# Kernel optimization log

Hardware: AMD Instinct MI355X
Metric: run time of the kernel (lower is better)

## Reference

```python
import jax, jax.numpy as jnp
import numpy as np
from jax import lax

EPS = 2e-5      # BatchNorm eps from source
TCLIP = 1.3     # FastSign STE clip


def fast_sign(x):
    # forward: sign(x); backward: grad of clamp(x, -1.3, 1.3) (straight-through)
    c = jnp.clip(x, -TCLIP, TCLIP)
    return lax.stop_gradient(jnp.sign(x) - c) + c


def conv2d(x, w, b, stride, pad):
    y = lax.conv_general_dilated(
        x, w, window_strides=stride,
        padding=[(pad[0], pad[0]), (pad[1], pad[1])],
        dimension_numbers=('NCHW', 'OIHW', 'NCHW'))
    return y + b[None, :, None, None]


def batchnorm(x, g, b):
    # training-mode BN: biased batch stats over (N, H, W)
    m = jnp.mean(x, axis=(0, 2, 3), keepdims=True)
    v = jnp.var(x, axis=(0, 2, 3), keepdims=True)
    return g[None, :, None, None] * (x - m) * lax.rsqrt(v + EPS) + b[None, :, None, None]


def maxpool3x3s2(x):
    return lax.reduce_window(x, -jnp.inf, lax.max, (1, 1, 3, 3), (1, 1, 2, 2), 'VALID')


def setup_inputs() -> dict:
    key = jax.random.key(0)
    ks = jax.random.split(key, 16)
    s = 0.05
    rn = lambda k, shape: jax.random.normal(k, shape, dtype=jnp.float32) * s
    NUM_CLASSES = 1000
    return {
        'x': jax.random.normal(ks[0], (8, 3, 211, 211), dtype=jnp.float32),
        'conv1_w': rn(ks[1], (96, 3, 11, 11)), 'conv1_b': rn(ks[2], (96,)),
        'bn1_g': jnp.ones((96,), jnp.float32), 'bn1_b': jnp.zeros((96,), jnp.float32),
        'conv2_w': rn(ks[3], (256, 96, 5, 5)), 'conv2_b': rn(ks[4], (256,)),
        'bn2_g': jnp.ones((256,), jnp.float32), 'bn2_b': jnp.zeros((256,), jnp.float32),
        'conv3_w': rn(ks[5], (384, 256, 3, 3)), 'conv3_b': rn(ks[6], (384,)),
        'bn3_g': jnp.ones((384,), jnp.float32), 'bn3_b': jnp.zeros((384,), jnp.float32),
        'conv4_w': rn(ks[7], (384, 384, 3, 3)), 'conv4_b': rn(ks[8], (384,)),
        'bn4_g': jnp.ones((384,), jnp.float32), 'bn4_b': jnp.zeros((384,), jnp.float32),
        'conv5_w': rn(ks[9], (256, 384, 3, 3)), 'conv5_b': rn(ks[10], (256,)),
        'bn5_g': jnp.ones((256,), jnp.float32), 'bn5_b': jnp.zeros((256,), jnp.float32),
        'fc1_w': rn(ks[11], (4096, 5)),
        'bn6_g': jnp.ones((256,), jnp.float32), 'bn6_b': jnp.zeros((256,), jnp.float32),
        'fc2_w': rn(ks[12], (4096, 4096)),
        'bn7_g': jnp.ones((256,), jnp.float32), 'bn7_b': jnp.zeros((256,), jnp.float32),
        'fc3_w': rn(ks[13], (NUM_CLASSES, 4096)), 'fc3_b': rn(ks[14], (NUM_CLASSES,)),
    }


def reference(x, conv1_w, conv1_b, bn1_g, bn1_b,
              conv2_w, conv2_b, bn2_g, bn2_b,
              conv3_w, conv3_b, bn3_g, bn3_b,
              conv4_w, conv4_b, bn4_g, bn4_b,
              conv5_w, conv5_b, bn5_g, bn5_b,
              fc1_w, bn6_g, bn6_b,
              fc2_w, bn7_g, bn7_b,
              fc3_w, fc3_b):
    # conv1 (full precision) + BN + relu + pool
    x = conv2d(x, conv1_w, conv1_b, (4, 4), (0, 0))           # [B,96,51,51]
    x = jax.nn.relu(batchnorm(x, bn1_g, bn1_b))
    x = maxpool3x3s2(x)                                        # [B,96,25,25]
    # binary conv blocks (act_q then BinaryConv2d binarizes input again, as in torch)
    x = fast_sign(x)
    x = conv2d(fast_sign(x), fast_sign(conv2_w), conv2_b, (1, 1), (2, 2))  # [B,256,25,25]
    x = batchnorm(x, bn2_g, bn2_b)
    x = maxpool3x3s2(x)                                        # [B,256,12,12]
    x = fast_sign(x)
    x = conv2d(fast_sign(x), fast_sign(conv3_w), conv3_b, (1, 1), (1, 1))  # [B,384,12,12]
    x = batchnorm(x, bn3_g, bn3_b)
    x = fast_sign(x)
    x = conv2d(fast_sign(x), fast_sign(conv4_w), conv4_b, (1, 1), (1, 1))
    x = batchnorm(x, bn4_g, bn4_b)
    x = fast_sign(x)
    x = conv2d(fast_sign(x), fast_sign(conv5_w), conv5_b, (1, 1), (1, 1))  # [B,256,12,12]
    x = batchnorm(x, bn5_g, bn5_b)
    x = maxpool3x3s2(x)                                        # [B,256,5,5]
    # fc layers applied on the LAST dim of the 4D tensor (faithful to torch F.linear)
    x = fast_sign(x)
    x = jnp.matmul(fast_sign(x), fast_sign(fc1_w).T)           # [B,256,5,4096]
    x = jax.nn.relu(batchnorm(x, bn6_g, bn6_b))
    x = fast_sign(x)
    x = jnp.matmul(fast_sign(x), fast_sign(fc2_w).T)           # [B,256,5,4096]
    x = jax.nn.relu(batchnorm(x, bn7_g, bn7_b))
    x = jnp.matmul(x, fc3_w.T) + fc3_b                         # [B,256,5,1000]
    return jax.nn.softmax(x, axis=1)                           # softmax over dim=1 (channels)
```

## Files before the change

### kernel.cpp

```cpp
#include <hip/hip_runtime.h>
#include <cstdint>
#include <cstddef>


typedef int      v4i  __attribute__((ext_vector_type(4)));
typedef float    v4f  __attribute__((ext_vector_type(4)));
typedef _Float16 v8h  __attribute__((ext_vector_type(8)));

#define EPS_BN 2e-5

__device__ __forceinline__ void g2l16(const void* g, void* l) {
  __builtin_amdgcn_global_load_lds((__attribute__((address_space(1))) void*)g,
                                   (__attribute__((address_space(3))) void*)l,
                                   16, 0, 0);
}

__global__ __launch_bounds__(256) void conv1_k(const float* __restrict__ x,
                                               const float* __restrict__ w,
                                               float* __restrict__ y) {
  const int bid = blockIdx.x;
  const int n = bid / 51, oh = bid % 51;
  const int tid = threadIdx.x, lane = tid & 63, wave = tid >> 6;
  __shared__ __align__(16) float xs[3 * 11 * 272];
  for (int i = tid; i < 3 * 11 * 272; i += 256) {
    int iw = i % 272;
    int t = i / 272;
    int kh = t % 11, ci = t / 11;
    float v = 0.f;
    if (iw < 211) v = x[((size_t)(n * 3 + ci) * 211 + (oh * 4 + kh)) * 211 + iw];
    xs[i] = v;
  }
  __syncthreads();
  const int ow = lane;
  const int g = blockIdx.y;
  {
    const int co0 = wave * 24 + g * 4;
    float a0 = 0.f, a1 = 0.f, a2 = 0.f, a3 = 0.f;
    for (int ci = 0; ci < 3; ++ci) {
#pragma unroll
      for (int kh = 0; kh < 11; ++kh) {
        const float* xr = xs + (ci * 11 + kh) * 272 + ow * 4;
        float4 q0 = *(const float4*)(xr);
        float4 q1 = *(const float4*)(xr + 4);
        float4 q2 = *(const float4*)(xr + 8);
        float xv[11] = {q0.x, q0.y, q0.z, q0.w, q1.x, q1.y,
                        q1.z, q1.w, q2.x, q2.y, q2.z};
        const float* wr = w + ((size_t)co0 * 3 + ci) * 121 + kh * 11;
#pragma unroll
        for (int kw = 0; kw < 11; ++kw) {
          float xvv = xv[kw];
          a0 = fmaf(xvv, wr[kw], a0);
          a1 = fmaf(xvv, wr[363 + kw], a1);
          a2 = fmaf(xvv, wr[726 + kw], a2);
          a3 = fmaf(xvv, wr[1089 + kw], a3);
        }
      }
    }
    if (ow < 51) {
      size_t ob = ((size_t)(n * 96 + co0) * 51 + oh) * 51 + ow;
      y[ob] = a0;
      y[ob + 2601] = a1;
      y[ob + 2 * 2601] = a2;
      y[ob + 3 * 2601] = a3;
    }
  }
}

template <typename T>
__global__ __launch_bounds__(256) void bnstat_nchw_k(const T* __restrict__ y,
                                                     const float* __restrict__ g,
                                                     const float* __restrict__ bb,
                                                     float* __restrict__ par,
                                                     int C, int HW, int Nn) {
  const int c = blockIdx.x;
  double s = 0.0, q = 0.0;
  for (int n = 0; n < Nn; ++n) {
    const T* p = y + ((size_t)n * C + c) * HW;
    for (int r = threadIdx.x; r < HW; r += 256) {
      double v = (double)p[r];
      s += v;
      q += v * v;
    }
  }
  __shared__ double ss[256], qq[256];
  ss[threadIdx.x] = s;
  qq[threadIdx.x] = q;
  __syncthreads();
  for (int st = 128; st > 0; st >>= 1) {
    if (threadIdx.x < st) {
      ss[threadIdx.x] += ss[threadIdx.x + st];
      qq[threadIdx.x] += qq[threadIdx.x + st];
    }
    __syncthreads();
  }
  if (threadIdx.x == 0) {
    double P = (double)Nn * HW;
    double m = ss[0] / P, var = qq[0] / P - m * m;
    float inv = (float)(1.0 / sqrt(var + EPS_BN));
    float sc = g[c] * inv;
    par[c] = sc;
    par[512 + c] = bb[c] - (float)m * sc;
  }
}

template <typename T>
__global__ __launch_bounds__(256) void bnstat_nhwc_k(const T* __restrict__ y,
                                                     const float* __restrict__ g,
                                                     const float* __restrict__ bb,
                                                     float* __restrict__ par,
                                                     int C, int P) {
  const int c = blockIdx.x;
  double s = 0.0, q = 0.0;
  for (int p = threadIdx.x; p < P; p += 256) {
    double v = (double)y[(size_t)p * C + c];
    s += v;
    q += v * v;
  }
  __shared__ double ss[256], qq[256];
  ss[threadIdx.x] = s;
  qq[threadIdx.x] = q;
  __syncthreads();
  for (int st = 128; st > 0; st >>= 1) {
    if (threadIdx.x < st) {
      ss[threadIdx.x] += ss[threadIdx.x + st];
      qq[threadIdx.x] += qq[threadIdx.x + st];
    }
    __syncthreads();
  }
  if (threadIdx.x == 0) {
    double Pd = (double)P;
    double m = ss[0] / Pd, var = qq[0] / Pd - m * m;
    float inv = (float)(1.0 / sqrt(var + EPS_BN));
    float sc = g[c] * inv;
    par[c] = sc;
    par[512 + c] = bb[c] - (float)m * sc;
  }
}

__global__ __launch_bounds__(256) void bnp16_k(const short* __restrict__ y,
                                               double* __restrict__ part) {
  const int c = blockIdx.x, n = blockIdx.y;
  const short* p = y + ((size_t)(n * 256 + c)) * 20480;
  long long s = 0, q = 0;
  for (int r = threadIdx.x; r < 20480; r += 256) {
    int v = p[r];
    s += v;
    q += (long long)v * v;
  }
  __shared__ long long ss[256], qq[256];
  ss[threadIdx.x] = s;
  qq[threadIdx.x] = q;
  __syncthreads();
  for (int st = 128; st > 0; st >>= 1) {
    if (threadIdx.x < st) {
      ss[threadIdx.x] += ss[threadIdx.x + st];
      qq[threadIdx.x] += qq[threadIdx.x + st];
    }
    __syncthreads();
  }
  if (threadIdx.x == 0) {
    part[(size_t)(n * 256 + c) * 2] = (double)ss[0];
    part[(size_t)(n * 256 + c) * 2 + 1] = (double)qq[0];
  }
}

__global__ __launch_bounds__(256) void bnf7_k(const double* __restrict__ part,
                                              const float* __restrict__ g,
                                              const float* __restrict__ bb,
                                              float* __restrict__ par) {
  int c = threadIdx.x;
  double s = 0.0, q = 0.0;
  for (int n = 0; n < 8; ++n) {
    s += part[(size_t)(n * 256 + c) * 2];
    q += part[(size_t)(n * 256 + c) * 2 + 1];
  }
  double P = 163840.0;
  double m = s / P, var = q / P - m * m;
  float inv = (float)(1.0 / sqrt(var + EPS_BN));
  float sc = g[c] * inv;
  par[c] = sc;
  par[512 + c] = bb[c] - (float)m * sc;
}

__global__ __launch_bounds__(256) void pool1sign_k(const float* __restrict__ y,
                                                   const float* __restrict__ par,
                                                   int8_t* __restrict__ o) {
  unsigned idx = blockIdx.x * 256 + threadIdx.x;
  if (idx >= 8u * 96 * 25 * 25) return;
  unsigned ow = idx % 25, t = idx / 25;
  unsigned oh = t % 25;
  t /= 25;
  unsigned c = t % 96, n = t / 96;
  float sc = par[c], sh = par[512 + c];
  const float* p = y + ((size_t)(n * 96 + c) * 51 + oh * 2) * 51 + ow * 2;
  float mx = -1e30f, mn = 1e30f;
#pragma unroll
  for (int kh = 0; kh < 3; ++kh)
#pragma unroll
    for (int kw = 0; kw < 3; ++kw) {
      float v = p[kh * 51 + kw];
      mx = fmaxf(mx, v);
      mn = fminf(mn, v);
    }
  float z = (sc >= 0.f ? sc * mx : sc * mn) + sh;
  o[((n * 25 + oh) * 25 + ow) * 96 + c] = (z > 0.f) ? 1 : 0;
}

__global__ __launch_bounds__(256) void poolsign_k(const short* __restrict__ y,
                                                  const float* __restrict__ par,
                                                  int8_t* __restrict__ o, int Nn,
                                                  int Hin, int C, int Hout) {
  unsigned idx = blockIdx.x * 256 + threadIdx.x;
  if (idx >= (unsigned)Nn * Hout * Hout * C) return;
  unsigned c = idx % C;
  unsigned t = idx / C;
  unsigned ow = t % Hout;
  t /= Hout;
  unsigned oh = t % Hout;
  unsigned n = t / Hout;
  const short* p = y + ((size_t)(n * Hin + oh * 2) * Hin + ow * 2) * C + c;
  int mx = -1000000, mn = 1000000;
#pragma unroll
  for (int kh = 0; kh < 3; ++kh)
#pragma unroll
    for (int kw = 0; kw < 3; ++kw) {
      int v = p[(kh * Hin + kw) * C];
      mx = max(mx, v);
      mn = min(mn, v);
    }
  float sc = par[c];
  float z = (sc >= 0.f ? sc * (float)mx : sc * (float)mn) + par[512 + c];
  o[idx] = (z > 0.f) ? 1 : ((z < 0.f) ? -1 : 0);
}

__global__ __launch_bounds__(256) void signk(const short* __restrict__ y,
                                             const float* __restrict__ par,
                                             int8_t* __restrict__ o, int total,
                                             int C) {
  unsigned idx = blockIdx.x * 256 + threadIdx.x;
  if (idx >= (unsigned)total) return;
  unsigned c = idx % C;
  float z = par[c] * (float)y[idx] + par[512 + c];
  o[idx] = (z > 0.f) ? 1 : ((z < 0.f) ? -1 : 0);
}

__global__ __launch_bounds__(256) void pool5sign_k(const short* __restrict__ y,
                                                   const float* __restrict__ par,
                                                   int8_t* __restrict__ o) {
  unsigned idx = blockIdx.x * 256 + threadIdx.x;
  if (idx >= 8u * 256 * 25) return;
  unsigned ow = idx % 5;
  unsigned t = idx / 5;
  unsigned oh = t % 5;
  t /= 5;
  unsigned c = t % 256, n = t / 256;
  const short* p = y + ((size_t)(n * 12 + oh * 2) * 12 + ow * 2) * 256 + c;
  int mx = -1000000, mn = 1000000;
#pragma unroll
  for (int kh = 0; kh < 3; ++kh)
#pragma unroll
    for (int kw = 0; kw < 3; ++kw) {
      int v = p[(kh * 12 + kw) * 256];
      mx = max(mx, v);
      mn = min(mn, v);
    }
  float sc = par[c];
  float z = (sc >= 0.f ? sc * (float)mx : sc * (float)mn) + par[512 + c];
  o[idx] = (z > 0.f) ? 1 : ((z < 0.f) ? -1 : 0);
}

__global__ __launch_bounds__(256) void quantw_k(const float* __restrict__ w,
                                                int8_t* __restrict__ o, int Co,
                                                int Ci, int KHW, int K, int Kp) {
  unsigned idx = blockIdx.x * 256 + threadIdx.x;
  if (idx >= (unsigned)Co * Kp) return;
  unsigned k = idx % Kp;
  unsigned co = idx / Kp;
  int8_t v = 0;
  if (k < (unsigned)K) {
    unsigned tap = k / Ci, ci = k - tap * Ci;
    float f = w[((size_t)co * Ci + ci) * KHW + tap];
    v = (f > 0.f) ? 1 : ((f < 0.f) ? -1 : 0);
  }
  o[idx] = v;
}

__global__ __launch_bounds__(256) void quantwv_k(const float* __restrict__ w,
                                                 int8_t* __restrict__ o,
                                                 unsigned total4) {
  unsigned idx = blockIdx.x * 256 + threadIdx.x;
  if (idx >= total4) return;
  float4 f = ((const float4*)w)[idx];
  union { int8_t b[4]; int i; } u;
  u.b[0] = (f.x > 0.f) ? 1 : ((f.x < 0.f) ? -1 : 0);
  u.b[1] = (f.y > 0.f) ? 1 : ((f.y < 0.f) ? -1 : 0);
  u.b[2] = (f.z > 0.f) ? 1 : ((f.z < 0.f) ? -1 : 0);
  u.b[3] = (f.w > 0.f) ? 1 : ((f.w < 0.f) ? -1 : 0);
  ((int*)o)[idx] = u.i;
}

__global__ __launch_bounds__(256) void im2colv_k(const int8_t* __restrict__ a,
                                                 int8_t* __restrict__ o, int Nn,
                                                 int H, int C, int KH, int pad,
                                                 int K, int Kp) {
  unsigned t = blockIdx.x * 256 + threadIdx.x;
  unsigned chunks = (unsigned)Kp >> 4;
  unsigned total = (unsigned)Nn * H * H * chunks;
  if (t >= total) return;
  unsigned kc = t % chunks;
  unsigned m = t / chunks;
  unsigned ow = m % H;
  unsigned tmp = m / H;
  unsigned oh = tmp % H;
  unsigned n = tmp / H;
  unsigned k0 = kc << 4;
  int4 v = {0, 0, 0, 0};
  if (k0 < (unsigned)K) {
    unsigned tap = k0 / C;
    unsigned ci = k0 - tap * C;
    unsigned kh = tap / KH, kw = tap - kh * KH;
    int ih = (int)oh - pad + (int)kh, iw = (int)ow - pad + (int)kw;
    if (ih >= 0 && ih < H && iw >= 0 && iw < H)
      v = *(const int4*)(a + (((n * H + ih) * H + iw) * C + ci));
  }
  *(int4*)(o + (size_t)m * Kp + k0) = v;
}

__global__ __launch_bounds__(256) void gemm_i8_k(const int8_t* __restrict__ A,
                                                 const int8_t* __restrict__ B,
                                                 short* __restrict__ Cm, int M,
                                                 int N, int Kp) {
  __shared__ __align__(16) int8_t As[128 * 64];
  __shared__ __align__(16) int8_t Bs[128 * 64];
  const int tid = threadIdx.x;
  const int lane = tid & 63, wave = tid >> 6;
  const int m0 = blockIdx.x * 128, n0 = blockIdx.y * 128;
  const int wm = (wave >> 1) * 64, wn = (wave & 1) * 64;
  v4i acc[4][4];
#pragma unroll
  for (int r = 0; r < 4; ++r)
#pragma unroll
    for (int u = 0; u < 4; ++u) acc[r][u] = (v4i){0, 0, 0, 0};

  int r_[2], g_[2];
#pragma unroll
  for (int q = 0; q < 2; ++q) {
    int idx = q * 256 + tid;
    r_[q] = idx >> 2;
    g_[q] = (((idx & 3) ^ ((r_[q] >> 1) & 3)) << 4);
  }
  int aoff[4], boff[4];
#pragma unroll
  for (int r = 0; r < 4; ++r) {
    int m = wm + r * 16 + (lane & 15);
    aoff[r] = m * 64 + (((lane >> 4) ^ ((m >> 1) & 3)) << 4);
    int n = wn + r * 16 + (lane & 15);
    boff[r] = n * 64 + (((lane >> 4) ^ ((n >> 1) & 3)) << 4);
  }

  for (int k0 = 0; k0 < Kp; k0 += 64) {
#pragma unroll
    for (int q = 0; q < 2; ++q) {
      int idx = q * 256 + tid;
      g2l16(A + (size_t)(m0 + r_[q]) * Kp + k0 + g_[q], As + idx * 16);
      g2l16(B + (size_t)(n0 + r_[q]) * Kp + k0 + g_[q], Bs + idx * 16);
    }
    __syncthreads();
    v4i af[4], bf[4];
#pragma unroll
    for (int r = 0; r < 4; ++r) {
      af[r] = *(const v4i*)(As + aoff[r]);
      bf[r] = *(const v4i*)(Bs + boff[r]);
    }
#pragma unroll
    for (int r = 0; r < 4; ++r)
#pragma unroll
      for (int u = 0; u < 4; ++u)
        acc[r][u] = __builtin_amdgcn_mfma_i32_16x16x64_i8(af[r], bf[u],
                                                          acc[r][u], 0, 0, 0);
    __syncthreads();
  }
  const int colD = lane & 15, rowD = (lane >> 4) * 4;
#pragma unroll
  for (int r = 0; r < 4; ++r)
#pragma unroll
    for (int u = 0; u < 4; ++u) {
      int n = n0 + wn + u * 16 + colD;
#pragma unroll
      for (int e = 0; e < 4; ++e) {
        int m = m0 + wm + r * 16 + rowD + e;
        if (m < M) Cm[(size_t)m * N + n] = (short)acc[r][u][e];
      }
    }
}

__global__ __launch_bounds__(256) void gemm_i8_64k(const int8_t* __restrict__ A,
                                                   const int8_t* __restrict__ B,
                                                   short* __restrict__ Cm, int M,
                                                   int N, int Kp) {
  __shared__ __align__(16) int8_t As[64 * 64];
  __shared__ __align__(16) int8_t Bs[64 * 64];
  const int tid = threadIdx.x;
  const int lane = tid & 63, wave = tid >> 6;
  const int m0 = blockIdx.x * 64, n0 = blockIdx.y * 64;
  const int wm = (wave >> 1) * 32, wn = (wave & 1) * 32;
  v4i acc[2][2];
#pragma unroll
  for (int r = 0; r < 2; ++r)
#pragma unroll
    for (int u = 0; u < 2; ++u) acc[r][u] = (v4i){0, 0, 0, 0};

  const int rs = tid >> 2;
  const int gsw = (((tid & 3) ^ ((rs >> 1) & 3)) << 4);
  int aoff[2], boff[2];
#pragma unroll
  for (int r = 0; r < 2; ++r) {
    int m = wm + r * 16 + (lane & 15);
    aoff[r] = m * 64 + (((lane >> 4) ^ ((m >> 1) & 3)) << 4);
    int n = wn + r * 16 + (lane & 15);
    boff[r] = n * 64 + (((lane >> 4) ^ ((n >> 1) & 3)) << 4);
  }

  for (int k0 = 0; k0 < Kp; k0 += 64) {
    g2l16(A + (size_t)(m0 + rs) * Kp + k0 + gsw, As + tid * 16);
    g2l16(B + (size_t)(n0 + rs) * Kp + k0 + gsw, Bs + tid * 16);
    __syncthreads();
    v4i af[2], bf[2];
#pragma unroll
    for (int r = 0; r < 2; ++r) {
      af[r] = *(const v4i*)(As + aoff[r]);
      bf[r] = *(const v4i*)(Bs + boff[r]);
    }
#pragma unroll
    for (int r = 0; r < 2; ++r)
#pragma unroll
      for (int u = 0; u < 2; ++u)
        acc[r][u] = __builtin_amdgcn_mfma_i32_16x16x64_i8(af[r], bf[u],
                                                          acc[r][u], 0, 0, 0);
    __syncthreads();
  }
  const int colD = lane & 15, rowD = (lane >> 4) * 4;
#pragma unroll
  for (int r = 0; r < 2; ++r)
#pragma unroll
    for (int u = 0; u < 2; ++u) {
      int n = n0 + wn + u * 16 + colD;
#pragma unroll
      for (int e = 0; e < 4; ++e) {
        int m = m0 + wm + r * 16 + rowD + e;
        if (m < M) Cm[(size_t)m * N + n] = (short)acc[r][u][e];
      }
    }
}

__global__ __launch_bounds__(256) void gemm_f16_k(const _Float16* __restrict__ A,
                                                  const _Float16* __restrict__ B,
                                                  float* __restrict__ out,
                                                  const float* __restrict__ bias,
                                                  int M, int Nout, int K) {
  __shared__ __align__(16) int8_t As[128 * 64];
  __shared__ __align__(16) int8_t Bs[128 * 64];
  const int tid = threadIdx.x;
  const int lane = tid & 63, wave = tid >> 6;
  const int m0 = blockIdx.x * 128, n0 = blockIdx.y * 128;
  const int wm = (wave >> 1) * 64, wn = (wave & 1) * 64;
  const int KpB = K * 2;
  v4f acc[4][4];
#pragma unroll
  for (int r = 0; r < 4; ++r)
#pragma unroll
    for (int u = 0; u < 4; ++u) acc[r][u] = (v4f){0.f, 0.f, 0.f, 0.f};

  int r_[2], g_[2];
#pragma unroll
  for (int q = 0; q < 2; ++q) {
    int idx = q * 256 + tid;
    r_[q] = idx >> 2;
    g_[q] = (((idx & 3) ^ ((r_[q] >> 1) & 3)) << 4);
  }
  int aoff[4], boff[4];
#pragma unroll
  for (int r = 0; r < 4; ++r) {
    int m = wm + r * 16 + (lane & 15);
    aoff[r] = m * 64 + (((lane >> 4) ^ ((m >> 1) & 3)) << 4);
    int n = wn + r * 16 + (lane & 15);
    boff[r] = n * 64 + (((lane >> 4) ^ ((n >> 1) & 3)) << 4);
  }

  const int8_t* Ab = (const int8_t*)A;
  const int8_t* Bb = (const int8_t*)B;
  for (int k0 = 0; k0 < KpB; k0 += 64) {
#pragma unroll
    for (int q = 0; q < 2; ++q) {
      int idx = q * 256 + tid;
      g2l16(Ab + (size_t)(m0 + r_[q]) * KpB + k0 + g_[q], As + idx * 16);
      g2l16(Bb + (size_t)(n0 + r_[q]) * KpB + k0 + g_[q], Bs + idx * 16);
    }
    __syncthreads();
    v8h af[4], bf[4];
#pragma unroll
    for (int r = 0; r < 4; ++r) {
      af[r] = *(const v8h*)(As + aoff[r]);
      bf[r] = *(const v8h*)(Bs + boff[r]);
    }
#pragma unroll
    for (int r = 0; r < 4; ++r)
#pragma unroll
      for (int u = 0; u < 4; ++u)
        acc[r][u] = __builtin_amdgcn_mfma_f32_16x16x32_f16(af[r], bf[u],
                                                           acc[r][u], 0, 0, 0);
    __syncthreads();
  }
  const int colD = lane & 15, rowD = (lane >> 4) * 4;
#pragma unroll
  for (int r = 0; r < 4; ++r)
#pragma unroll
    for (int u = 0; u < 4; ++u) {
      int n = n0 + wn + u * 16 + colD;
      if (n < Nout) {
        float bv = bias[n];
#pragma unroll
        for (int e = 0; e < 4; ++e) {
          int m = m0 + wm + r * 16 + rowD + e;
          if (m < M) out[(size_t)m * Nout + n] = acc[r][u][e] + bv;
        }
      }
    }
}

__global__ __launch_bounds__(256) void gram_k(const int8_t* __restrict__ wq1,
                                              int* __restrict__ gm) {
  __shared__ int sg[30];
  if (threadIdx.x < 30) sg[threadIdx.x] = 0;
  __syncthreads();
  int acc[30];
#pragma unroll
  for (int i = 0; i < 30; ++i) acc[i] = 0;
  for (int j = threadIdx.x; j < 4096; j += 256) {
    const int8_t* w = wq1 + j * 5;
    int v[5];
#pragma unroll
    for (int k = 0; k < 5; ++k) v[k] = w[k];
#pragma unroll
    for (int k = 0; k < 5; ++k) {
      acc[k] += v[k];
#pragma unroll
      for (int l = 0; l < 5; ++l) acc[5 + k * 5 + l] += v[k] * v[l];
    }
  }
#pragma unroll
  for (int i = 0; i < 30; ++i) atomicAdd(&sg[i], acc[i]);
  __syncthreads();
  if (threadIdx.x < 30) gm[threadIdx.x] = sg[threadIdx.x];
}

__global__ __launch_bounds__(256) void par6_k(const int8_t* __restrict__ s5,
                                              const int* __restrict__ gm,
                                              const float* __restrict__ g,
                                              const float* __restrict__ bb,
                                              float* __restrict__ par) {
  int c = threadIdx.x;
  long long s = 0, q = 0;
  for (int n = 0; n < 8; ++n)
    for (int i = 0; i < 5; ++i) {
      const int8_t* a = s5 + ((size_t)((n * 256 + c) * 5 + i)) * 5;
      int av[5];
#pragma unroll
      for (int k = 0; k < 5; ++k) av[k] = a[k];
      int ds = 0, dq = 0;
#pragma unroll
      for (int k = 0; k < 5; ++k) {
        ds += av[k] * gm[k];
#pragma unroll
        for (int l = 0; l < 5; ++l) dq += av[k] * av[l] * gm[5 + k * 5 + l];
      }
      s += ds;
      q += dq;
    }
  double P = 163840.0;
  double m = (double)s / P, var = (double)q / P - m * m;
  float inv = (float)(1.0 / sqrt(var + EPS_BN));
  float sc = g[c] * inv;
  par[c] = sc;
  par[512 + c] = bb[c] - (float)m * sc;
}

__global__ __launch_bounds__(256) void fc1f_k(const int8_t* __restrict__ s5,
                                              const int8_t* __restrict__ wq1,
                                              const float* __restrict__ par,
                                              int8_t* __restrict__ f1) {
  unsigned idx = blockIdx.x * 256 + threadIdx.x;
  if (idx >= 10240u * 256) return;
  unsigned m = idx >> 8, jg = idx & 255;
  unsigned c = (m / 5) & 255;
  float sc = par[c], sh = par[512 + c];
  const int8_t* ap = s5 + m * 5;
  int a0 = ap[0], a1 = ap[1], a2 = ap[2], a3 = ap[3], a4 = ap[4];
  int8_t wb[80];
  const int4* wp = (const int4*)(wq1 + jg * 80);
#pragma unroll
  for (int qq = 0; qq < 5; ++qq) *(int4*)(wb + qq * 16) = wp[qq];
  union { int8_t b[16]; int4 v; } ov;
#pragma unroll
  for (int t = 0; t < 16; ++t) {
    int d = a0 * wb[t * 5] + a1 * wb[t * 5 + 1] + a2 * wb[t * 5 + 2] +
            a3 * wb[t * 5 + 3] + a4 * wb[t * 5 + 4];
    float z = sc * (float)d + sh;
    ov.b[t] = (z > 0.f) ? 1 : 0;
  }
  *(int4*)(f1 + (size_t)m * 4096 + jg * 16) = ov.v;
}

__global__ __launch_bounds__(256) void x7v_k(short* __restrict__ f2,
                                             const float* __restrict__ par) {
  unsigned idx = blockIdx.x * 256 + threadIdx.x;
  if (idx >= 10240u * 4096 / 8) return;
  unsigned base8 = idx * 8;
  unsigned c = (base8 / 20480) & 255;
  float sc = par[c], sh = par[512 + c];
  union { int4 v; short s[8]; } in;
  in.v = *(int4*)(f2 + (size_t)base8);
  union { int4 v; _Float16 h[8]; } outv;
#pragma unroll
  for (int t = 0; t < 8; ++t) {
    float z = sc * (float)in.s[t] + sh;
    if (z < 0.f) z = 0.f;
    outv.h[t] = (_Float16)z;
  }
  *(int4*)((_Float16*)f2 + (size_t)base8) = outv.v;
}

__global__ __launch_bounds__(256) void w3h_k(const float* __restrict__ w,
                                             _Float16* __restrict__ o) {
  unsigned idx = blockIdx.x * 256 + threadIdx.x;
  if (idx >= 1024u * 4096) return;
  unsigned j = idx >> 12;
  o[idx] = (j < 1000) ? (_Float16)w[idx] : (_Float16)0.f;
}

__global__ __launch_bounds__(256) void softmax_k(float* __restrict__ o) {
  unsigned t = blockIdx.x * 256 + threadIdx.x;
  if (t >= 40000) return;
  unsigned j = t % 1000;
  unsigned i = (t / 1000) % 5;
  unsigned b = t / 5000;
  float* p = o + ((size_t)(b * 256) * 5 + i) * 1000 + j;
  float mx = -1e30f;
  for (int c = 0; c < 256; ++c) mx = fmaxf(mx, p[(size_t)c * 5000]);
  float s = 0.f;
  for (int c = 0; c < 256; ++c) s += expf(p[(size_t)c * 5000] - mx);
  float inv = 1.f / s;
  for (int c = 0; c < 256; ++c)
    p[(size_t)c * 5000] = expf(p[(size_t)c * 5000] - mx) * inv;
}

static inline unsigned gs(size_t n) { return (unsigned)((n + 255) / 256); }

extern "C" void kernel_launch(void* const* d_in, const int* in_sizes, int n_in,
                              void* d_out, int out_size, void* d_ws,
                              size_t ws_size, hipStream_t stream) {
  (void)in_sizes; (void)n_in; (void)out_size; (void)ws_size;
  const float* x    = (const float*)d_in[0];
  const float* w1   = (const float*)d_in[1];
  const float* bn1g = (const float*)d_in[3];
  const float* bn1b = (const float*)d_in[4];
  const float* w2   = (const float*)d_in[5];
  const float* bn2g = (const float*)d_in[7];
  const float* bn2b = (const float*)d_in[8];
  const float* w3   = (const float*)d_in[9];
  const float* bn3g = (const float*)d_in[11];
  const float* bn3b = (const float*)d_in[12];
  const float* w4   = (const float*)d_in[13];
  const float* bn4g = (const float*)d_in[15];
  const float* bn4b = (const float*)d_in[16];
  const float* w5   = (const float*)d_in[17];
  const float* bn5g = (const float*)d_in[19];
  const float* bn5b = (const float*)d_in[20];
  const float* fc1w = (const float*)d_in[21];
  const float* bn6g = (const float*)d_in[22];
  const float* bn6b = (const float*)d_in[23];
  const float* fc2w = (const float*)d_in[24];
  const float* bn7g = (const float*)d_in[25];
  const float* bn7b = (const float*)d_in[26];
  const float* fc3w = (const float*)d_in[27];
  const float* fc3b = (const float*)d_in[28];
  float* out = (float*)d_out;

  char* ws = (char*)d_ws;
  size_t off = 0;
  auto alloc = [&](size_t bytes) -> void* {
    off = (off + 255) & ~(size_t)255;
    void* p = ws + off;
    off += bytes;
    return p;
  };
  float*   Y1   = (float*)alloc((size_t)8 * 96 * 51 * 51 * 4);
  int8_t*  S1   = (int8_t*)alloc((size_t)8 * 25 * 25 * 96);
  int8_t*  IM   = (int8_t*)alloc((size_t)5120 * 2432);
  short*   Y2   = (short*)alloc((size_t)5056 * 256 * 2);
  int8_t*  S2   = (int8_t*)alloc((size_t)1152 * 256);
  short*   Y3   = (short*)alloc((size_t)1152 * 384 * 2);
  int8_t*  S3   = (int8_t*)alloc((size_t)1152 * 384);
  short*   Y4   = (short*)alloc((size_t)1152 * 384 * 2);
  int8_t*  S4   = (int8_t*)alloc((size_t)1152 * 384);
  short*   Y5   = (short*)alloc((size_t)1152 * 256 * 2);
  int8_t*  S5   = (int8_t*)alloc((size_t)8 * 256 * 25);
  int8_t*  WQ2  = (int8_t*)alloc((size_t)256 * 2432);
  int8_t*  WQ3  = (int8_t*)alloc((size_t)384 * 2304);
  int8_t*  WQ4  = (int8_t*)alloc((size_t)384 * 3456);
  int8_t*  WQ5  = (int8_t*)alloc((size_t)256 * 3456);
  int8_t*  WQ1  = (int8_t*)alloc((size_t)4096 * 5);
  int8_t*  WQF2 = (int8_t*)alloc((size_t)4096 * 4096);
  int8_t*  F1   = (int8_t*)alloc((size_t)10240 * 4096);
  short*   F2   = (short*)alloc((size_t)10240 * 4096 * 2);
  _Float16* W3H = (_Float16*)alloc((size_t)1024 * 4096 * 2);
  float*   PAR  = (float*)alloc((size_t)7 * 1024 * 4);
  int*     GM   = (int*)alloc(32 * 4);
  double*  PART = (double*)alloc((size_t)2048 * 2 * 8);
  float* par1 = PAR;
  float* par2 = PAR + 1024;
  float* par3 = PAR + 2048;
  float* par4 = PAR + 3072;
  float* par5 = PAR + 4096;
  float* par6 = PAR + 5120;
  float* par7 = PAR + 6144;

  quantw_k<<<gs((size_t)256 * 2432), 256, 0, stream>>>(w2, WQ2, 256, 96, 25, 2400, 2432);
  quantw_k<<<gs((size_t)384 * 2304), 256, 0, stream>>>(w3, WQ3, 384, 256, 9, 2304, 2304);
  quantw_k<<<gs((size_t)384 * 3456), 256, 0, stream>>>(w4, WQ4, 384, 384, 9, 3456, 3456);
  quantw_k<<<gs((size_t)256 * 3456), 256, 0, stream>>>(w5, WQ5, 256, 384, 9, 3456, 3456);
  quantw_k<<<gs((size_t)4096 * 5), 256, 0, stream>>>(fc1w, WQ1, 4096, 5, 1, 5, 5);
  quantwv_k<<<gs((size_t)4096 * 1024), 256, 0, stream>>>(fc2w, WQF2, 4096u * 1024);
  w3h_k<<<gs((size_t)1024 * 4096), 256, 0, stream>>>(fc3w, W3H);

  conv1_k<<<dim3(8 * 51, 6), 256, 0, stream>>>(x, w1, Y1);
  bnstat_nchw_k<float><<<dim3(96), 256, 0, stream>>>(Y1, bn1g, bn1b, par1, 96, 2601, 8);
  pool1sign_k<<<gs((size_t)8 * 96 * 625), 256, 0, stream>>>(Y1, par1, S1);

  im2colv_k<<<gs((size_t)5000 * 152), 256, 0, stream>>>(S1, IM, 8, 25, 96, 5, 2, 2400, 2432);
  gemm_i8_64k<<<dim3(79, 4), 256, 0, stream>>>(IM, WQ2, Y2, 5000, 256, 2432);
  bnstat_nhwc_k<short><<<dim3(256), 256, 0, stream>>>(Y2, bn2g, bn2b, par2, 256, 5000);
  poolsign_k<<<gs((size_t)8 * 144 * 256), 256, 0, stream>>>(Y2, par2, S2, 8, 25, 256, 12);

  im2colv_k<<<gs((size_t)1152 * 144), 256, 0, stream>>>(S2, IM, 8, 12, 256, 3, 1, 2304, 2304);
  gemm_i8_64k<<<dim3(18, 6), 256, 0, stream>>>(IM, WQ3, Y3, 1152, 384, 2304);
  bnstat_nhwc_k<short><<<dim3(384), 256, 0, stream>>>(Y3, bn3g, bn3b, par3, 384, 1152);
  signk<<<gs((size_t)1152 * 384), 256, 0, stream>>>(Y3, par3, S3, 1152 * 384, 384);

  im2colv_k<<<gs((size_t)1152 * 216), 256, 0, stream>>>(S3, IM, 8, 12, 384, 3, 1, 3456, 3456);
  gemm_i8_64k<<<dim3(18, 6), 256, 0, stream>>>(IM, WQ4, Y4, 1152, 384, 3456);
  bnstat_nhwc_k<short><<<dim3(384), 256, 0, stream>>>(Y4, bn4g, bn4b, par4, 384, 1152);
  signk<<<gs((size_t)1152 * 384), 256, 0, stream>>>(Y4, par4, S4, 1152 * 384, 384);

  im2colv_k<<<gs((size_t)1152 * 216), 256, 0, stream>>>(S4, IM, 8, 12, 384, 3, 1, 3456, 3456);
  gemm_i8_64k<<<dim3(18, 4), 256, 0, stream>>>(IM, WQ5, Y5, 1152, 256, 3456);
  bnstat_nhwc_k<short><<<dim3(256), 256, 0, stream>>>(Y5, bn5g, bn5b, par5, 256, 1152);
  pool5sign_k<<<gs((size_t)8 * 256 * 25), 256, 0, stream>>>(Y5, par5, S5);

  gram_k<<<dim3(1), 256, 0, stream>>>(WQ1, GM);
  par6_k<<<dim3(1), 256, 0, stream>>>(S5, GM, bn6g, bn6b, par6);
  fc1f_k<<<gs((size_t)10240 * 256), 256, 0, stream>>>(S5, WQ1, par6, F1);

  gemm_i8_k<<<dim3(80, 32), 256, 0, stream>>>(F1, WQF2, F2, 10240, 4096, 4096);
  bnp16_k<<<dim3(256, 8), 256, 0, stream>>>(F2, PART);
  bnf7_k<<<dim3(1), 256, 0, stream>>>(PART, bn7g, bn7b, par7);
  x7v_k<<<gs((size_t)10240 * 512), 256, 0, stream>>>(F2, par7);

  gemm_f16_k<<<dim3(80, 8), 256, 0, stream>>>((const _Float16*)F2, W3H, out, fc3b,
                                              10240, 1000, 4096);
  softmax_k<<<gs(40000), 256, 0, stream>>>(out);
}
```

Before: 1.099 ms.

## Split-K conv3-5 GEMMs with fused slice reduction and tile softmax in LDS

Result: faster. 0.9996 ms (-9.1%).

```diff
diff --git a/kernel.cpp b/kernel.cpp
--- a/kernel.cpp
+++ b/kernel.cpp
@@ -103,18 +103,20 @@
   }
 }
 
-template <typename T>
-__global__ __launch_bounds__(256) void bnstat_nhwc_k(const T* __restrict__ y,
+__global__ __launch_bounds__(256) void bnstat_nhwc_k(const short* __restrict__ y,
                                                      const float* __restrict__ g,
                                                      const float* __restrict__ bb,
                                                      float* __restrict__ par,
-                                                     int C, int P) {
+                                                     int C, int P, int S) {
   const int c = blockIdx.x;
   double s = 0.0, q = 0.0;
+  const size_t MN = (size_t)P * C;
   for (int p = threadIdx.x; p < P; p += 256) {
-    double v = (double)y[(size_t)p * C + c];
-    s += v;
-    q += v * v;
+    int v = 0;
+    for (int sl = 0; sl < S; ++sl) v += y[sl * MN + (size_t)p * C + c];
+    double dv = (double)v;
+    s += dv;
+    q += dv * dv;
   }
   __shared__ double ss[256], qq[256];
   ss[threadIdx.x] = s;
@@ -236,17 +238,19 @@
 __global__ __launch_bounds__(256) void signk(const short* __restrict__ y,
                                              const float* __restrict__ par,
                                              int8_t* __restrict__ o, int total,
-                                             int C) {
+                                             int C, int S) {
   unsigned idx = blockIdx.x * 256 + threadIdx.x;
   if (idx >= (unsigned)total) return;
   unsigned c = idx % C;
-  float z = par[c] * (float)y[idx] + par[512 + c];
+  int v = 0;
+  for (int sl = 0; sl < S; ++sl) v += y[(size_t)sl * total + idx];
+  float z = par[c] * (float)v + par[512 + c];
   o[idx] = (z > 0.f) ? 1 : ((z < 0.f) ? -1 : 0);
 }
 
 __global__ __launch_bounds__(256) void pool5sign_k(const short* __restrict__ y,
                                                    const float* __restrict__ par,
-                                                   int8_t* __restrict__ o) {
+                                                   int8_t* __restrict__ o, int S) {
   unsigned idx = blockIdx.x * 256 + threadIdx.x;
   if (idx >= 8u * 256 * 25) return;
   unsigned ow = idx % 5;
@@ -254,13 +258,15 @@
   unsigned oh = t % 5;
   t /= 5;
   unsigned c = t % 256, n = t / 256;
+  const size_t MN = (size_t)1152 * 256;
   const short* p = y + ((size_t)(n * 12 + oh * 2) * 12 + ow * 2) * 256 + c;
   int mx = -1000000, mn = 1000000;
 #pragma unroll
   for (int kh = 0; kh < 3; ++kh)
 #pragma unroll
     for (int kw = 0; kw < 3; ++kw) {
-      int v = p[(kh * 12 + kw) * 256];
+      int v = 0;
+      for (int sl = 0; sl < S; ++sl) v += p[sl * MN + (kh * 12 + kw) * 256];
       mx = max(mx, v);
       mn = min(mn, v);
     }
@@ -397,19 +403,21 @@
 __global__ __launch_bounds__(256) void gemm_i8_64k(const int8_t* __restrict__ A,
                                                    const int8_t* __restrict__ B,
                                                    short* __restrict__ Cm, int M,
-                                                   int N, int Kp) {
+                                                   int N, int Kp, int Kslice) {
   __shared__ __align__(16) int8_t As[64 * 64];
   __shared__ __align__(16) int8_t Bs[64 * 64];
   const int tid = threadIdx.x;
   const int lane = tid & 63, wave = tid >> 6;
   const int m0 = blockIdx.x * 64, n0 = blockIdx.y * 64;
+  const int kbeg = blockIdx.z * Kslice;
+  const int kend = min(kbeg + Kslice, Kp);
+  v4i acc[2][2];
+#pragma unroll
+  for (int r = 0; r < 2; ++r)
+#pragma unroll
+    for (int u = 0; u < 2; ++u) acc[r][u] = (v4i){0, 0, 0, 0};
+
   const int wm = (wave >> 1) * 32, wn = (wave & 1) * 32;
-  v4i acc[2][2];
-#pragma unroll
-  for (int r = 0; r < 2; ++r)
-#pragma unroll
-    for (int u = 0; u < 2; ++u) acc[r][u] = (v4i){0, 0, 0, 0};
-
   const int rs = tid >> 2;
   const int gsw = (((tid & 3) ^ ((rs >> 1) & 3)) << 4);
   int aoff[2], boff[2];
@@ -421,7 +429,7 @@
     boff[r] = n * 64 + (((lane >> 4) ^ ((n >> 1) & 3)) << 4);
   }
 
-  for (int k0 = 0; k0 < Kp; k0 += 64) {
+  for (int k0 = kbeg; k0 < kend; k0 += 64) {
     g2l16(A + (size_t)(m0 + rs) * Kp + k0 + gsw, As + tid * 16);
     g2l16(B + (size_t)(n0 + rs) * Kp + k0 + gsw, Bs + tid * 16);
     __syncthreads();
@@ -439,6 +447,7 @@
                                                           acc[r][u], 0, 0, 0);
     __syncthreads();
   }
+  short* Cz = Cm + (size_t)blockIdx.z * M * N;
   const int colD = lane & 15, rowD = (lane >> 4) * 4;
 #pragma unroll
   for (int r = 0; r < 2; ++r)
@@ -448,7 +457,7 @@
 #pragma unroll
       for (int e = 0; e < 4; ++e) {
         int m = m0 + wm + r * 16 + rowD + e;
-        if (m < M) Cm[(size_t)m * N + n] = (short)acc[r][u][e];
+        if (m < M) Cz[(size_t)m * N + n] = (short)acc[r][u][e];
       }
     }
 }
@@ -639,19 +648,52 @@
 }
 
 __global__ __launch_bounds__(256) void softmax_k(float* __restrict__ o) {
-  unsigned t = blockIdx.x * 256 + threadIdx.x;
-  if (t >= 40000) return;
-  unsigned j = t % 1000;
-  unsigned i = (t / 1000) % 5;
-  unsigned b = t / 5000;
-  float* p = o + ((size_t)(b * 256) * 5 + i) * 1000 + j;
-  float mx = -1e30f;
-  for (int c = 0; c < 256; ++c) mx = fmaxf(mx, p[(size_t)c * 5000]);
-  float s = 0.f;
-  for (int c = 0; c < 256; ++c) s += expf(p[(size_t)c * 5000] - mx);
-  float inv = 1.f / s;
-  for (int c = 0; c < 256; ++c)
-    p[(size_t)c * 5000] = expf(p[(size_t)c * 5000] - mx) * inv;
+  __shared__ float tile[256][33];
+  __shared__ float red[8][32];
+  __shared__ float mxs[32], invs[32];
+  const int bi = blockIdx.x;
+  const int jt = blockIdx.y;
+  const int b = bi / 5, i = bi % 5;
+  float* base = o + ((size_t)(b * 256) * 5 + i) * 1000;
+  const int t = threadIdx.x;
+  const int jl = t & 31, part = t >> 5;
+  const int j = jt * 32 + jl;
+  const bool ok = (j < 1000);
+  for (int cg = 0; cg < 32; ++cg) {
+    int c = cg * 8 + part;
+    tile[c][jl] = ok ? base[(size_t)c * 5000 + j] : 0.f;
+  }
+  __syncthreads();
+  float pm = -1e30f;
+#pragma unroll 4
+  for (int cc = 0; cc < 32; ++cc) pm = fmaxf(pm, tile[part * 32 + cc][jl]);
+  red[part][jl] = pm;
+  __syncthreads();
+  if (part == 0) {
+    float m = red[0][jl];
+#pragma unroll
+    for (int p = 1; p < 8; ++p) m = fmaxf(m, red[p][jl]);
+    mxs[jl] = m;
+  }
+  __syncthreads();
+  float mx = mxs[jl];
+  float ps = 0.f;
+#pragma unroll 4
+  for (int cc = 0; cc < 32; ++cc) ps += expf(tile[part * 32 + cc][jl] - mx);
+  red[part][jl] = ps;
+  __syncthreads();
+  if (part == 0) {
+    float s = red[0][jl];
+#pragma unroll
+    for (int p = 1; p < 8; ++p) s += red[p][jl];
+    invs[jl] = 1.f / s;
+  }
+  __syncthreads();
+  float inv = invs[jl];
+  for (int cg = 0; cg < 32; ++cg) {
+    int c = cg * 8 + part;
+    if (ok) base[(size_t)c * 5000 + j] = expf(tile[c][jl] - mx) * inv;
+  }
 }
 
 static inline unsigned gs(size_t n) { return (unsigned)((n + 255) / 256); }
@@ -699,11 +741,11 @@
   int8_t*  IM   = (int8_t*)alloc((size_t)5120 * 2432);
   short*   Y2   = (short*)alloc((size_t)5056 * 256 * 2);
   int8_t*  S2   = (int8_t*)alloc((size_t)1152 * 256);
-  short*   Y3   = (short*)alloc((size_t)1152 * 384 * 2);
+  short*   Y3   = (short*)alloc((size_t)1152 * 384 * 2 * 4);
   int8_t*  S3   = (int8_t*)alloc((size_t)1152 * 384);
-  short*   Y4   = (short*)alloc((size_t)1152 * 384 * 2);
+  short*   Y4   = (short*)alloc((size_t)1152 * 384 * 2 * 3);
   int8_t*  S4   = (int8_t*)alloc((size_t)1152 * 384);
-  short*   Y5   = (short*)alloc((size_t)1152 * 256 * 2);
+  short*   Y5   = (short*)alloc((size_t)1152 * 256 * 2 * 3);
   int8_t*  S5   = (int8_t*)alloc((size_t)8 * 256 * 25);
   int8_t*  WQ2  = (int8_t*)alloc((size_t)256 * 2432);
   int8_t*  WQ3  = (int8_t*)alloc((size_t)384 * 2304);
@@ -738,24 +780,24 @@
   pool1sign_k<<<gs((size_t)8 * 96 * 625), 256, 0, stream>>>(Y1, par1, S1);
 
   im2colv_k<<<gs((size_t)5000 * 152), 256, 0, stream>>>(S1, IM, 8, 25, 96, 5, 2, 2400, 2432);
-  gemm_i8_64k<<<dim3(79, 4), 256, 0, stream>>>(IM, WQ2, Y2, 5000, 256, 2432);
-  bnstat_nhwc_k<short><<<dim3(256), 256, 0, stream>>>(Y2, bn2g, bn2b, par2, 256, 5000);
+  gemm_i8_64k<<<dim3(79, 4, 1), 256, 0, stream>>>(IM, WQ2, Y2, 5000, 256, 2432, 2432);
+  bnstat_nhwc_k<<<dim3(256), 256, 0, stream>>>(Y2, bn2g, bn2b, par2, 256, 5000, 1);
   poolsign_k<<<gs((size_t)8 * 144 * 256), 256, 0, stream>>>(Y2, par2, S2, 8, 25, 256, 12);
 
   im2colv_k<<<gs((size_t)1152 * 144), 256, 0, stream>>>(S2, IM, 8, 12, 256, 3, 1, 2304, 2304);
-  gemm_i8_64k<<<dim3(18, 6), 256, 0, stream>>>(IM, WQ3, Y3, 1152, 384, 2304);
-  bnstat_nhwc_k<short><<<dim3(384), 256, 0, stream>>>(Y3, bn3g, bn3b, par3, 384, 1152);
-  signk<<<gs((size_t)1152 * 384), 256, 0, stream>>>(Y3, par3, S3, 1152 * 384, 384);
+  gemm_i8_64k<<<dim3(18, 6, 4), 256, 0, stream>>>(IM, WQ3, Y3, 1152, 384, 2304, 576);
+  bnstat_nhwc_k<<<dim3(384), 256, 0, stream>>>(Y3, bn3g, bn3b, par3, 384, 1152, 4);
+  signk<<<gs((size_t)1152 * 384), 256, 0, stream>>>(Y3, par3, S3, 1152 * 384, 384, 4);
 
   im2colv_k<<<gs((size_t)1152 * 216), 256, 0, stream>>>(S3, IM, 8, 12, 384, 3, 1, 3456, 3456);
-  gemm_i8_64k<<<dim3(18, 6), 256, 0, stream>>>(IM, WQ4, Y4, 1152, 384, 3456);
-  bnstat_nhwc_k<short><<<dim3(384), 256, 0, stream>>>(Y4, bn4g, bn4b, par4, 384, 1152);
-  signk<<<gs((size_t)1152 * 384), 256, 0, stream>>>(Y4, par4, S4, 1152 * 384, 384);
+  gemm_i8_64k<<<dim3(18, 6, 3), 256, 0, stream>>>(IM, WQ4, Y4, 1152, 384, 3456, 1152);
+  bnstat_nhwc_k<<<dim3(384), 256, 0, stream>>>(Y4, bn4g, bn4b, par4, 384, 1152, 3);
+  signk<<<gs((size_t)1152 * 384), 256, 0, stream>>>(Y4, par4, S4, 1152 * 384, 384, 3);
 
   im2colv_k<<<gs((size_t)1152 * 216), 256, 0, stream>>>(S4, IM, 8, 12, 384, 3, 1, 3456, 3456);
-  gemm_i8_64k<<<dim3(18, 4), 256, 0, stream>>>(IM, WQ5, Y5, 1152, 256, 3456);
-  bnstat_nhwc_k<short><<<dim3(256), 256, 0, stream>>>(Y5, bn5g, bn5b, par5, 256, 1152);
-  pool5sign_k<<<gs((size_t)8 * 256 * 25), 256, 0, stream>>>(Y5, par5, S5);
+  gemm_i8_64k<<<dim3(18, 4, 3), 256, 0, stream>>>(IM, WQ5, Y5, 1152, 256, 3456, 1152);
+  bnstat_nhwc_k<<<dim3(256), 256, 0, stream>>>(Y5, bn5g, bn5b, par5, 256, 1152, 3);
+  pool5sign_k<<<gs((size_t)8 * 256 * 25), 256, 0, stream>>>(Y5, par5, S5, 3);
 
   gram_k<<<dim3(1), 256, 0, stream>>>(WQ1, GM);
   par6_k<<<dim3(1), 256, 0, stream>>>(S5, GM, bn6g, bn6b, par6);
@@ -768,5 +810,5 @@
 
   gemm_f16_k<<<dim3(80, 8), 256, 0, stream>>>((const _Float16*)F2, W3H, out, fc3b,
                                               10240, 1000, 4096);
-  softmax_k<<<gs(40000), 256, 0, stream>>>(out);
-}
+  softmax_k<<<dim3(40, 32), 256, 0, stream>>>(out);
+}
```
